# Performance work log

Hardware: AMD Instinct MI355X
Metric: run time of the kernel (lower is better)

The kernel has to match this reference:

```python
import jax, jax.numpy as jnp
import numpy as np
import math

N_NODES, N_EDGES, NNZ, D, L = 100000, 20000, 500000, 128, 4
ALPHA, LAMDA = 0.1, 0.5


def setup_inputs() -> dict:
    key = jax.random.key(0)
    ks = jax.random.split(key, 16)
    x = jax.random.normal(ks[0], (N_NODES, D), jnp.float32)
    e = jax.random.normal(ks[1], (N_EDGES, D), jnp.float32)
    nodes = jax.random.randint(ks[2], (NNZ,), 0, N_NODES)
    edges = jnp.sort(jax.random.randint(ks[3], (NNZ,), 0, N_EDGES)).at[-1].set(N_EDGES - 1)
    hyperedge_index = jnp.stack([nodes, edges]).astype(jnp.int32)
    dist_v2e = jax.random.randint(ks[4], (NNZ,), 0, 64).astype(jnp.float32)
    deg_v2e = jax.random.randint(ks[5], (NNZ,), 0, 64).astype(jnp.float32)
    dist_e2v = jax.random.randint(ks[6], (NNZ,), 0, 64).astype(jnp.float32)
    deg_e2v = jax.random.randint(ks[7], (NNZ,), 0, 64).astype(jnp.float32)
    s = 0.05
    W0 = jax.random.normal(ks[8], (D, D), jnp.float32) * s
    b0 = jnp.zeros((D,), jnp.float32)
    Wn = jax.random.normal(ks[9], (L, D, D), jnp.float32) * s
    We = jax.random.normal(ks[10], (L, D, D), jnp.float32) * s
    attn_w = jax.random.normal(ks[11], (L, 2 * D), jnp.float32) * s
    attn_b = jnp.zeros((L,), jnp.float32)
    wd_w = jax.random.normal(ks[12], (L,), jnp.float32) * s
    wd_b = jnp.zeros((L,), jnp.float32)
    wg_w = jax.random.normal(ks[13], (L,), jnp.float32) * s
    wg_b = jnp.zeros((L,), jnp.float32)
    return dict(x=x, e=e, hyperedge_index=hyperedge_index, dist_v2e=dist_v2e,
                deg_v2e=deg_v2e, dist_e2v=dist_e2v, deg_e2v=deg_e2v,
                W0=W0, b0=b0, Wn=Wn, We=We, attn_w=attn_w, attn_b=attn_b,
                wd_w=wd_w, wd_b=wd_b, wg_w=wg_w, wg_b=wg_b)


def _seg_softmax(s, idx, num):
    # numerically-stable scatter_softmax over segments idx
    m = jax.ops.segment_max(s, idx, num_segments=num)
    ex = jnp.exp(s - m[idx])
    den = jax.ops.segment_sum(ex, idx, num_segments=num)
    return ex / den[idx]


def _forward(x, e, hei, dv2e, gv2e, de2v, ge2v, W0, b0, Wn, We, aw, ab, wdw, wdb, wgw, wgb):
    nodes, edges = hei[0], hei[1]
    N, E = x.shape[0], e.shape[0]
    ones = jnp.ones(nodes.shape[0], x.dtype)
    dV = jax.ops.segment_sum(ones, nodes, num_segments=N)
    cnt = jax.ops.segment_sum(ones, edges, num_segments=E)
    dE = jax.ops.segment_sum(dV[nodes], edges, num_segments=E) / jnp.maximum(cnt, 1.0)
    degV = jnp.where(dV > 0, dV ** -0.5, 1.0)[:, None]   # [N,1]
    degE = jnp.where(dE > 0, dE ** -0.5, 1.0)[:, None]   # [E,1]

    x = jax.nn.relu(x @ W0 + b0)
    x0, e0 = x, e
    d = x.shape[1]
    for i in range(L):
        beta = math.log(LAMDA / (i + 1) + 1.0)
        # v2e attention: concat [x[nodes], e[edges]] -> softmax over edge segments
        sx1 = x @ aw[i, :d]; se1 = e @ aw[i, d:]
        s_v2e = sx1[nodes] + se1[edges] + ab[i] + dv2e * wdw[i] + wdb[i] + gv2e * wgw[i] + wgb[i]
        a_v2e = _seg_softmax(s_v2e, edges, E)[:, None]
        # e2v attention (flipped): concat [e[edges], x[nodes]] -> softmax over node segments
        se2 = e @ aw[i, :d]; sx2 = x @ aw[i, d:]
        s_e2v = se2[edges] + sx2[nodes] + ab[i] + de2v * wdw[i] + wdb[i] + ge2v * wgw[i] + wgb[i]
        a_e2v = _seg_softmax(s_e2v, nodes, N)[:, None]

        Xe1 = jax.ops.segment_sum(x[nodes] * a_v2e, edges, num_segments=E) * degE
        Xv1 = jax.ops.segment_sum(Xe1[edges] * a_e2v, nodes, num_segments=N) * degV
        Xv2 = jax.ops.segment_sum(e[edges] * a_e2v, nodes, num_segments=N) * degV
        Xe2 = jax.ops.segment_sum(Xv2[nodes] * a_v2e, edges, num_segments=E) * degE
        xm = (Xv1 + Xv2) * 0.5
        em = (Xe1 + Xe2) * 0.5
        xi = (1 - ALPHA) * xm + ALPHA * x0
        x = (1 - beta) * xi + beta * (xi @ Wn[i])
        ei = (1 - ALPHA) * em + ALPHA * e0
        e = (1 - beta) * ei + beta * (ei @ We[i])
        if i < L - 1:
            x = jax.nn.relu(x)
            e = jax.nn.relu(e)
    return x, e


def reference(x, e, hyperedge_index, dist_v2e, deg_v2e, dist_e2v, deg_e2v,
              W0, b0, Wn, We, attn_w, attn_b, wd_w, wd_b, wg_w, wg_b):
    return _forward(x, e, hyperedge_index, dist_v2e, deg_v2e, dist_e2v, deg_e2v,
                    W0, b0, Wn, We, attn_w, attn_b, wd_w, wd_b, wg_w, wg_b)
```

## Files before the change

kernel.cpp:

```cpp
#include <hip/hip_runtime.h>
#include <hip/hip_fp16.h>
#include <math.h>

#define DD 128
#define SCAN_BLOCKS 256

typedef _Float16 f16x8 __attribute__((ext_vector_type(8)));
typedef float f32x4 __attribute__((ext_vector_type(4)));

__device__ inline float wave_sum(float v){
#pragma unroll
  for (int m = 32; m >= 1; m >>= 1) v += __shfl_xor(v, m, 64);
  return v;
}
__device__ inline int wave_sum_i(int v){
#pragma unroll
  for (int m = 32; m >= 1; m >>= 1) v += __shfl_xor(v, m, 64);
  return v;
}


__global__ void k_edge_offsets(const int* __restrict__ edges, int nnz, int E,
                               int* __restrict__ eo){
  int e = blockIdx.x * blockDim.x + threadIdx.x;
  if (e > E) return;
  int lo = 0, hi = nnz;
  while (lo < hi){ int mid = (lo + hi) >> 1; if (edges[mid] < e) lo = mid + 1; else hi = mid; }
  eo[e] = lo;
}

__global__ void k_hist(const int* __restrict__ nodes, int nnz, int* __restrict__ dV){
  int k = blockIdx.x * blockDim.x + threadIdx.x;
  if (k < nnz) atomicAdd(&dV[nodes[k]], 1);
}

__global__ __launch_bounds__(256) void k_scan_partial(const int* __restrict__ dV, int N,
                                                      int* __restrict__ part){
  int b = blockIdx.x, t = threadIdx.x;
  int chunk = (N + SCAN_BLOCKS - 1) / SCAN_BLOCKS;
  int s0 = b * chunk, s1 = min(s0 + chunk, N);
  int sum = 0;
  for (int n = s0 + t; n < s1; n += 256) sum += dV[n];
  sum = wave_sum_i(sum);
  __shared__ int wred[4];
  int lane = t & 63, wid = t >> 6;
  if (lane == 0) wred[wid] = sum;
  __syncthreads();
  if (t == 0) part[b] = wred[0] + wred[1] + wred[2] + wred[3];
}

__global__ __launch_bounds__(SCAN_BLOCKS) void k_scan_blocksums(int* __restrict__ part){
  __shared__ int sh[SCAN_BLOCKS];
  int t = threadIdx.x;
  int v = part[t];
  sh[t] = v; __syncthreads();
  for (int off = 1; off < SCAN_BLOCKS; off <<= 1){
    int add = (t >= off) ? sh[t - off] : 0;
    __syncthreads();
    sh[t] += add;
    __syncthreads();
  }
  part[t] = sh[t] - v;
}

__global__ __launch_bounds__(256) void k_scan_apply(const int* __restrict__ dV, int N, int nnz,
    const int* __restrict__ partScan, int* __restrict__ no, int* __restrict__ nfill,
    float* __restrict__ degV){
  int b = blockIdx.x, t = threadIdx.x;
  int chunk = (N + SCAN_BLOCKS - 1) / SCAN_BLOCKS;
  int s0 = b * chunk, s1 = min(s0 + chunk, N);
  int lane = t & 63, wid = t >> 6;
  __shared__ int wtot[4];
  __shared__ int s_run;
  if (t == 0) s_run = partScan[b];
  __syncthreads();
  for (int base = s0; base < s1; base += 256){
    int n = base + t;
    int d = (n < s1) ? dV[n] : 0;
    int v = d;
#pragma unroll
    for (int off = 1; off < 64; off <<= 1){
      int o = __shfl_up(v, off, 64);
      if (lane >= off) v += o;
    }
    if (lane == 63) wtot[wid] = v;
    __syncthreads();
    int run0 = s_run;
    int woff = 0;
    for (int w = 0; w < wid; w++) woff += wtot[w];
    if (n < s1){
      int excl = run0 + woff + v - d;
      no[n] = excl; nfill[n] = excl;
      degV[n] = d > 0 ? 1.0f / sqrtf((float)d) : 1.0f;
    }
    int btot = wtot[0] + wtot[1] + wtot[2] + wtot[3];
    __syncthreads();
    if (t == 0) s_run = run0 + btot;
    __syncthreads();
  }
  if (b == 0 && t == 0) no[N] = nnz;
}

__global__ void k_perm(const int* __restrict__ nodes, int nnz,
                       int* __restrict__ nfill, int* __restrict__ perm){
  int k = blockIdx.x * blockDim.x + threadIdx.x;
  if (k < nnz){ int pos = atomicAdd(&nfill[nodes[k]], 1); perm[pos] = k; }
}

__global__ void k_pack(const int* __restrict__ perm, const int* __restrict__ edges,
                       const float* __restrict__ dist, const float* __restrict__ deg,
                       int nnz, float4* __restrict__ pack){
  int j = blockIdx.x * blockDim.x + threadIdx.x;
  if (j < nnz){
    int k = perm[j];
    pack[j] = make_float4(__int_as_float(edges[k]), dist[k], deg[k], 0.f);
  }
}

__global__ void k_edge_deg(const int* __restrict__ nodes, const int* __restrict__ eo, int E,
                           const int* __restrict__ dV, float* __restrict__ degE){
  int e = blockIdx.x * blockDim.x + threadIdx.x;
  if (e >= E) return;
  int b = eo[e], en = eo[e + 1];
  float s = 0.f;
  for (int k = b; k < en; k++) s += (float)dV[nodes[k]];
  float cnt = (float)(en - b);
  float dE = s / fmaxf(cnt, 1.0f);
  degE[e] = dE > 0.f ? 1.0f / sqrtf(dE) : 1.0f;
}

__global__ void k_tohalf(const float2* __restrict__ src, __half2* __restrict__ dst, int n){
  int i = blockIdx.x * blockDim.x + threadIdx.x;
  if (i < n){ float2 v = src[i]; dst[i] = __floats2half2_rn(v.x, v.y); }
}

__global__ __launch_bounds__(256) void k_einit(const float2* __restrict__ e_in2,
    const float* __restrict__ aw1, const float* __restrict__ aw2,
    int E, __half2* __restrict__ ET, float* __restrict__ se1, float* __restrict__ se2){
  int wave = threadIdx.x >> 6, lane = threadIdx.x & 63;
  int e = blockIdx.x * 4 + wave;
  if (e >= E) return;
  float2 v = e_in2[(size_t)e * 64 + lane];
  ET[(size_t)e * 128 + 2 * lane + 1] = __floats2half2_rn(v.x, v.y);
  float2 a2v = ((const float2*)aw2)[lane];
  float2 a1v = ((const float2*)aw1)[lane];
  float s1 = v.x * a2v.x + v.y * a2v.y;
  float s2 = v.x * a1v.x + v.y * a1v.y;
  s1 = wave_sum(s1); s2 = wave_sum(s2);
  if (lane == 0){ se1[e] = s1; se2[e] = s2; }
}

__global__ void k_wcast(const float* __restrict__ W0, const float* __restrict__ Wn,
                        const float* __restrict__ We, _Float16* __restrict__ Wt){
  int idx = blockIdx.x * 256 + threadIdx.x;
  if (idx >= 9 * 16384) return;
  int m = idx >> 14, r = idx & 16383;
  int n = r >> 7, k = r & 127;
  const float* src = (m == 0) ? W0 : (m <= 4 ? Wn + (size_t)(m - 1) * 16384
                                             : We + (size_t)(m - 5) * 16384);
  Wt[(size_t)m * 16384 + n * 128 + k] = (_Float16)src[k * 128 + n];
}


__global__ __launch_bounds__(256) void k_softmax_v2e(
    const int* __restrict__ nodes, const int* __restrict__ eo,
    const float* __restrict__ sx1, const float* __restrict__ se1,
    const float* __restrict__ dist, const float* __restrict__ deg,
    const float* __restrict__ ab, const float* __restrict__ wdw, const float* __restrict__ wdb,
    const float* __restrict__ wgw, const float* __restrict__ wgb, int li,
    const float* __restrict__ degE,
    int E, float* __restrict__ a_out, float* __restrict__ esc){
  int l32 = threadIdx.x & 31;
  int grp = threadIdx.x >> 5;
  int e = blockIdx.x * 8 + grp;
  if (e >= E) return;
  int b = eo[e], en = eo[e + 1];
  if (b >= en){ if (l32 == 0) esc[e] = 0.f; return; }
  float base = se1[e] + ab[li] + wdb[li] + wgb[li];
  float wd = wdw[li], wg = wgw[li];
  float m = -INFINITY;
  for (int k = b + l32; k < en; k += 32){
    float s = sx1[nodes[k]] + base + dist[k] * wd + deg[k] * wg;
    a_out[k] = s;
    m = fmaxf(m, s);
  }
#pragma unroll
  for (int mm = 16; mm >= 1; mm >>= 1) m = fmaxf(m, __shfl_xor(m, mm, 32));
  float sum = 0.f;
  for (int k = b + l32; k < en; k += 32){
    float ex = expf(a_out[k] - m);
    a_out[k] = ex; sum += ex;
  }
#pragma unroll
  for (int mm = 16; mm >= 1; mm >>= 1) sum += __shfl_xor(sum, mm, 32);
  if (l32 == 0) esc[e] = degE[e] / sum;
}

__device__ inline void acc8h(const float4 q, float w, float* a){
  float2 h0 = __half22float2(*(const __half2*)&q.x);
  float2 h1 = __half22float2(*(const __half2*)&q.y);
  float2 h2v = __half22float2(*(const __half2*)&q.z);
  float2 h3 = __half22float2(*(const __half2*)&q.w);
  a[0] += w * h0.x; a[1] += w * h0.y; a[2] += w * h1.x; a[3] += w * h1.y;
  a[4] += w * h2v.x; a[5] += w * h2v.y; a[6] += w * h3.x; a[7] += w * h3.y;
}

__global__ __launch_bounds__(256) void k_agg1(const int* __restrict__ nodes, const int* __restrict__ eo,
    const float4* __restrict__ xh4, const float* __restrict__ a_v2e, const float* __restrict__ esc,
    int E, __half2* __restrict__ ET){
  int l32 = threadIdx.x & 31;
  int grp = threadIdx.x >> 5;
  int e = blockIdx.x * 8 + grp;
  if (e >= E) return;
  int b = eo[e], en = eo[e + 1];
  int l16 = l32 & 15, hf = l32 >> 4;
  float a[8] = {0.f, 0.f, 0.f, 0.f, 0.f, 0.f, 0.f, 0.f};
  int k = b + hf;
  for (; k + 2 < en; k += 4){
    int n0 = nodes[k], n1 = nodes[k + 2];
    float w0 = a_v2e[k], w1 = a_v2e[k + 2];
    float4 v0 = xh4[(size_t)n0 * 16 + l16];
    float4 v1 = xh4[(size_t)n1 * 16 + l16];
    acc8h(v0, w0, a); acc8h(v1, w1, a);
  }
  for (; k < en; k += 2){
    int n = nodes[k];
    float w = a_v2e[k];
    float4 v = xh4[(size_t)n * 16 + l16];
    acc8h(v, w, a);
  }
#pragma unroll
  for (int j = 0; j < 8; j++) a[j] += __shfl_xor(a[j], 16, 32);
  if (hf == 0){
    float s = esc[e];
    size_t o = (size_t)e * 128 + 8 * l16;
    ET[o]     = __floats2half2_rn(a[0] * s, a[1] * s);
    ET[o + 2] = __floats2half2_rn(a[2] * s, a[3] * s);
    ET[o + 4] = __floats2half2_rn(a[4] * s, a[5] * s);
    ET[o + 6] = __floats2half2_rn(a[6] * s, a[7] * s);
  }
}

__device__ inline void acc8(const float4 q, float w, float* a1, float* a2){
  float2 x0 = __half22float2(*(const __half2*)&q.x);
  float2 e0 = __half22float2(*(const __half2*)&q.y);
  float2 x1 = __half22float2(*(const __half2*)&q.z);
  float2 e1 = __half22float2(*(const __half2*)&q.w);
  a1[0] += w * x0.x; a1[1] += w * x0.y; a1[2] += w * x1.x; a1[3] += w * x1.y;
  a2[0] += w * e0.x; a2[1] += w * e0.y; a2[2] += w * e1.x; a2[3] += w * e1.y;
}

__global__ __launch_bounds__(256) void k_agg2f(
    const float4* __restrict__ pack, const int* __restrict__ no,
    const float* __restrict__ se2, const float* __restrict__ sx2,
    const float* __restrict__ ab, const float* __restrict__ wdw, const float* __restrict__ wdb,
    const float* __restrict__ wgw, const float* __restrict__ wgb, int li,
    const float4* __restrict__ ETq,
    const float* __restrict__ degV, const __half2* __restrict__ x0h,
    int N, __half2* __restrict__ Xv2h, float* __restrict__ xi){
  int l32 = threadIdx.x & 31;
  int grp = threadIdx.x >> 5;
  int n = blockIdx.x * 8 + grp;
  if (n >= N) return;
  int b = no[n], en = no[n + 1];
  float base = sx2[n] + ab[li] + wdb[li] + wgb[li];
  float wd = wdw[li], wg = wgw[li];
  float m_run = -INFINITY, l_run = 0.f;
  float a1[4] = {0.f, 0.f, 0.f, 0.f}, a2[4] = {0.f, 0.f, 0.f, 0.f};
  for (int cb = b; cb < en; cb += 32){
    int cs = min(32, en - cb);
    float s = -INFINITY; int e_l = 0;
    if (l32 < cs){
      float4 pk = pack[cb + l32];
      e_l = __float_as_int(pk.x);
      s = se2[e_l] + base + pk.y * wd + pk.z * wg;
    }
    float m_c = s;
#pragma unroll
    for (int mm = 16; mm >= 1; mm >>= 1) m_c = fmaxf(m_c, __shfl_xor(m_c, mm, 32));
    float p = (l32 < cs) ? expf(s - m_c) : 0.f;
    float l_c = p;
#pragma unroll
    for (int mm = 16; mm >= 1; mm >>= 1) l_c += __shfl_xor(l_c, mm, 32);
    float m_new = fmaxf(m_run, m_c);
    float f_old = expf(m_run - m_new);
    float f_c = expf(m_c - m_new);
#pragma unroll
    for (int r = 0; r < 4; r++){ a1[r] *= f_old; a2[r] *= f_old; }
    l_run = l_run * f_old + l_c * f_c;
    m_run = m_new;
    int jj = 0;
    for (; jj + 3 < cs; jj += 4){
      float w0 = __shfl(p, jj, 32) * f_c;
      float w1 = __shfl(p, jj + 1, 32) * f_c;
      float w2 = __shfl(p, jj + 2, 32) * f_c;
      float w3 = __shfl(p, jj + 3, 32) * f_c;
      int e0i = __shfl(e_l, jj, 32);
      int e1i = __shfl(e_l, jj + 1, 32);
      int e2i = __shfl(e_l, jj + 2, 32);
      int e3i = __shfl(e_l, jj + 3, 32);
      float4 q0 = ETq[(size_t)e0i * 32 + l32];
      float4 q1 = ETq[(size_t)e1i * 32 + l32];
      float4 q2 = ETq[(size_t)e2i * 32 + l32];
      float4 q3 = ETq[(size_t)e3i * 32 + l32];
      acc8(q0, w0, a1, a2);
      acc8(q1, w1, a1, a2);
      acc8(q2, w2, a1, a2);
      acc8(q3, w3, a1, a2);
    }
    for (; jj < cs; jj++){
      float w = __shfl(p, jj, 32) * f_c;
      int ei_ = __shfl(e_l, jj, 32);
      float4 q = ETq[(size_t)ei_ * 32 + l32];
      acc8(q, w, a1, a2);
    }
  }
  float inv = l_run > 0.f ? 1.0f / l_run : 0.f;
  float dv = degV[n] * inv;
  float2 st;
  *(__half2*)&st.x = __floats2half2_rn(a2[0] * dv, a2[1] * dv);
  *(__half2*)&st.y = __floats2half2_rn(a2[2] * dv, a2[3] * dv);
  *(float2*)&Xv2h[(size_t)n * 64 + 2 * l32] = st;
  float2 x0v2 = *(const float2*)&x0h[(size_t)n * 64 + 2 * l32];
  float2 h0 = __half22float2(*(const __half2*)&x0v2.x);
  float2 h1 = __half22float2(*(const __half2*)&x0v2.y);
  float4 o;
  o.x = 0.45f * dv * (a1[0] + a2[0]) + 0.1f * h0.x;
  o.y = 0.45f * dv * (a1[1] + a2[1]) + 0.1f * h0.y;
  o.z = 0.45f * dv * (a1[2] + a2[2]) + 0.1f * h1.x;
  o.w = 0.45f * dv * (a1[3] + a2[3]) + 0.1f * h1.y;
  *(float4*)(xi + (size_t)n * 128 + 4 * l32) = o;
}

__global__ __launch_bounds__(256) void k_agg3(const int* __restrict__ nodes, const int* __restrict__ eo,
    const float4* __restrict__ Xv2h4, const float* __restrict__ a_v2e, const float* __restrict__ esc,
    const float4* __restrict__ ETq, const float* __restrict__ e0,
    int E, float* __restrict__ ei){
  int l32 = threadIdx.x & 31;
  int grp = threadIdx.x >> 5;
  int e = blockIdx.x * 8 + grp;
  if (e >= E) return;
  int b = eo[e], en = eo[e + 1];
  int l16 = l32 & 15, hf = l32 >> 4;
  float a[8] = {0.f, 0.f, 0.f, 0.f, 0.f, 0.f, 0.f, 0.f};
  int k = b + hf;
  for (; k + 2 < en; k += 4){
    int n0 = nodes[k], n1 = nodes[k + 2];
    float w0 = a_v2e[k], w1 = a_v2e[k + 2];
    float4 v0 = Xv2h4[(size_t)n0 * 16 + l16];
    float4 v1 = Xv2h4[(size_t)n1 * 16 + l16];
    acc8h(v0, w0, a); acc8h(v1, w1, a);
  }
  for (; k < en; k += 2){
    int n = nodes[k];
    float w = a_v2e[k];
    float4 v = Xv2h4[(size_t)n * 16 + l16];
    acc8h(v, w, a);
  }
#pragma unroll
  for (int j = 0; j < 8; j++) a[j] += __shfl_xor(a[j], 16, 32);
  if (hf == 0){
    float dE = esc[e];
    float4 q0 = ETq[(size_t)e * 32 + 2 * l16];
    float4 q1 = ETq[(size_t)e * 32 + 2 * l16 + 1];
    float2 x01 = __half22float2(*(const __half2*)&q0.x);
    float2 x23 = __half22float2(*(const __half2*)&q0.z);
    float2 x45 = __half22float2(*(const __half2*)&q1.x);
    float2 x67 = __half22float2(*(const __half2*)&q1.z);
    const float4* e04 = (const float4*)(e0 + (size_t)e * 128 + 8 * l16);
    float4 ev0 = e04[0], ev1 = e04[1];
    float4 o0, o1;
    o0.x = 0.45f * (x01.x + a[0] * dE) + 0.1f * ev0.x;
    o0.y = 0.45f * (x01.y + a[1] * dE) + 0.1f * ev0.y;
    o0.z = 0.45f * (x23.x + a[2] * dE) + 0.1f * ev0.z;
    o0.w = 0.45f * (x23.y + a[3] * dE) + 0.1f * ev0.w;
    o1.x = 0.45f * (x45.x + a[4] * dE) + 0.1f * ev1.x;
    o1.y = 0.45f * (x45.y + a[5] * dE) + 0.1f * ev1.y;
    o1.z = 0.45f * (x67.x + a[6] * dE) + 0.1f * ev1.z;
    o1.w = 0.45f * (x67.y + a[7] * dE) + 0.1f * ev1.w;
    float* eip = ei + (size_t)e * 128 + 8 * l16;
    *(float4*)eip = o0;
    *(float4*)(eip + 4) = o1;
  }
}

__global__ __launch_bounds__(256) void k_gemm_mfma(
    const _Float16* __restrict__ Ah, const _Float16* __restrict__ Wt,
    const float* __restrict__ Af, const float* __restrict__ bias,
    float* __restrict__ outf, _Float16* __restrict__ outh, _Float16* __restrict__ outh2, int et,
    const float* __restrict__ awA, const float* __restrict__ awB,
    float* __restrict__ sA, float* __restrict__ sB,
    int nrows, float beta, int mode, int do_relu){
  int wave = threadIdx.x >> 6, lane = threadIdx.x & 63;
  int row0 = blockIdx.x * 64 + wave * 16;
  if (row0 >= nrows) return;
  int lm = lane & 15;
  int lk8 = (lane >> 4) * 8;
  int arow = row0 + lm; if (arow >= nrows) arow = nrows - 1;
  f16x8 afrag[4];
  if (mode == 0){
#pragma unroll
    for (int ks = 0; ks < 4; ks++)
      afrag[ks] = *(const f16x8*)(Ah + (size_t)arow * 128 + ks * 32 + lk8);
  } else {
    const float* ap = Af + (size_t)arow * 128;
#pragma unroll
    for (int ks = 0; ks < 4; ks++){
      float4 v0 = *(const float4*)(ap + ks * 32 + lk8);
      float4 v1 = *(const float4*)(ap + ks * 32 + lk8 + 4);
      f16x8 a;
      a[0] = (_Float16)v0.x; a[1] = (_Float16)v0.y; a[2] = (_Float16)v0.z; a[3] = (_Float16)v0.w;
      a[4] = (_Float16)v1.x; a[5] = (_Float16)v1.y; a[6] = (_Float16)v1.z; a[7] = (_Float16)v1.w;
      afrag[ks] = a;
    }
  }
  int rbase = (lane >> 4) * 4;
  float da[4] = {0.f, 0.f, 0.f, 0.f}, db[4] = {0.f, 0.f, 0.f, 0.f};
  for (int t = 0; t < 8; t++){
    f32x4 acc = {0.f, 0.f, 0.f, 0.f};
#pragma unroll
    for (int ks = 0; ks < 4; ks++){
      f16x8 bf = *(const f16x8*)(Wt + (size_t)(t * 16 + lm) * 128 + ks * 32 + lk8);
      acc = __builtin_amdgcn_mfma_f32_16x16x32_f16(afrag[ks], bf, acc, 0, 0, 0);
    }
    int col = t * 16 + lm;
    float wa = 0.f, wb = 0.f;
    if (awA){ wa = awA[col]; wb = awB[col]; }
#pragma unroll
    for (int r = 0; r < 4; r++){
      int gr = row0 + rbase + r;
      if (gr >= nrows) continue;
      float v;
      if (mode == 0) v = acc[r] + bias[col];
      else v = (1.0f - beta) * Af[(size_t)gr * 128 + col] + beta * acc[r];
      if (do_relu) v = fmaxf(v, 0.f);
      if (outf) outf[(size_t)gr * 128 + col] = v;
      if (outh){
        if (et) outh[(size_t)gr * 256 + (col >> 1) * 4 + 2 + (col & 1)] = (_Float16)v;
        else    outh[(size_t)gr * 128 + col] = (_Float16)v;
      }
      if (outh2) outh2[(size_t)gr * 128 + col] = (_Float16)v;
      da[r] += v * wa; db[r] += v * wb;
    }
  }
  if (awA){
#pragma unroll
    for (int r = 0; r < 4; r++){
      float a = da[r], bb = db[r];
#pragma unroll
      for (int m = 8; m >= 1; m >>= 1){
        a += __shfl_xor(a, m, 64);
        bb += __shfl_xor(bb, m, 64);
      }
      int gr = row0 + rbase + r;
      if (lm == 0 && gr < nrows){ sA[gr] = a; sB[gr] = bb; }
    }
  }
}


extern "C" void kernel_launch(void* const* d_in, const int* in_sizes, int n_in,
                              void* d_out, int out_size, void* d_ws, size_t ws_size,
                              hipStream_t stream) {
  const float* x_in     = (const float*)d_in[0];
  const float* e_in     = (const float*)d_in[1];
  const int*   hei      = (const int*)d_in[2];
  const float* dist_v2e = (const float*)d_in[3];
  const float* deg_v2e  = (const float*)d_in[4];
  const float* dist_e2v = (const float*)d_in[5];
  const float* deg_e2v  = (const float*)d_in[6];
  const float* W0       = (const float*)d_in[7];
  const float* b0       = (const float*)d_in[8];
  const float* Wn       = (const float*)d_in[9];
  const float* We       = (const float*)d_in[10];
  const float* attn_w   = (const float*)d_in[11];
  const float* attn_b   = (const float*)d_in[12];
  const float* wd_w     = (const float*)d_in[13];
  const float* wd_b     = (const float*)d_in[14];
  const float* wg_w     = (const float*)d_in[15];
  const float* wg_b     = (const float*)d_in[16];

  const int N   = in_sizes[0] / DD;
  const int E   = in_sizes[1] / DD;
  const int NNZ = in_sizes[2] / 2;
  const int* nodesArr = hei;
  const int* edgesArr = hei + NNZ;

  float* out_x = (float*)d_out;
  float* out_e = (float*)d_out + (size_t)N * DD;

  __half2* Xv2h = (__half2*)out_x;
  __half2* xh   = (__half2*)((char*)out_x + (size_t)N * DD * 2);
  __half2* ET   = (__half2*)out_e;
  const float4* ETq = (const float4*)out_e;

  char* wsp = (char*)d_ws;
  auto alloc = [&](size_t bytes) -> void* {
    void* p = (void*)wsp;
    wsp += (bytes + 255) / 256 * 256;
    return p;
  };
  float* xS1   = (float*)alloc((size_t)N * DD * 4);
  float* eS1   = (float*)alloc((size_t)E * DD * 4);
  _Float16* xinh = (_Float16*)alloc((size_t)N * DD * 2);
  _Float16* x0h  = (_Float16*)alloc((size_t)N * DD * 2);
  _Float16* Wt   = (_Float16*)alloc((size_t)9 * 16384 * 2);
  float* sx1   = (float*)alloc((size_t)N * 4);
  float* sx2   = (float*)alloc((size_t)N * 4);
  float* se1   = (float*)alloc((size_t)E * 4);
  float* se2   = (float*)alloc((size_t)E * 4);
  float* a_v2e = (float*)alloc((size_t)NNZ * 4);
  float* degV  = (float*)alloc((size_t)N * 4);
  float* degE  = (float*)alloc((size_t)E * 4);
  float* esc   = (float*)alloc((size_t)E * 4);
  float4* pack = (float4*)alloc((size_t)NNZ * 16);
  int* dV_i  = (int*)alloc((size_t)N * 4);
  int* no_   = (int*)alloc((size_t)(N + 1) * 4);
  int* nfill = (int*)alloc((size_t)N * 4);
  int* perm  = (int*)alloc((size_t)NNZ * 4);
  int* eo    = (int*)alloc((size_t)(E + 1) * 4);
  int* part  = (int*)alloc((size_t)SCAN_BLOCKS * 4);

  hipMemsetAsync(dV_i, 0, (size_t)N * 4, stream);
  k_edge_offsets<<<(E + 1 + 255) / 256, 256, 0, stream>>>(edgesArr, NNZ, E, eo);
  k_hist<<<(NNZ + 255) / 256, 256, 0, stream>>>(nodesArr, NNZ, dV_i);
  k_scan_partial<<<SCAN_BLOCKS, 256, 0, stream>>>(dV_i, N, part);
  k_scan_blocksums<<<1, SCAN_BLOCKS, 0, stream>>>(part);
  k_scan_apply<<<SCAN_BLOCKS, 256, 0, stream>>>(dV_i, N, NNZ, part, no_, nfill, degV);
  k_perm<<<(NNZ + 255) / 256, 256, 0, stream>>>(nodesArr, NNZ, nfill, perm);
  k_pack<<<(NNZ + 255) / 256, 256, 0, stream>>>(perm, edgesArr, dist_e2v, deg_e2v, NNZ, pack);
  k_edge_deg<<<(E + 255) / 256, 256, 0, stream>>>(nodesArr, eo, E, dV_i, degE);
  k_wcast<<<(9 * 16384 + 255) / 256, 256, 0, stream>>>(W0, Wn, We, Wt);

  const float* aw1_0 = attn_w;
  const float* aw2_0 = attn_w + 128;

  k_einit<<<(E + 3) / 4, 256, 0, stream>>>((const float2*)e_in, aw1_0, aw2_0,
                                            E, ET, se1, se2);
  k_tohalf<<<((N * 64) + 255) / 256, 256, 0, stream>>>((const float2*)x_in, (__half2*)xinh, N * 64);

  k_gemm_mfma<<<(N + 63) / 64, 256, 0, stream>>>(xinh, Wt, nullptr, b0,
      nullptr, (_Float16*)xh, x0h, 0, aw1_0, aw2_0, sx1, sx2, N, 0.f, 0, 1);

  for (int i = 0; i < 4; i++){
    float beta = logf(0.5f / (float)(i + 1) + 1.0f);
    const float* aw1n = (i < 3) ? attn_w + (size_t)(i + 1) * 256        : nullptr;
    const float* aw2n = (i < 3) ? attn_w + (size_t)(i + 1) * 256 + 128  : nullptr;

    k_softmax_v2e<<<(E + 7) / 8, 256, 0, stream>>>(nodesArr, eo, sx1, se1,
        dist_v2e, deg_v2e, attn_b, wd_w, wd_b, wg_w, wg_b, i, degE, E, a_v2e, esc);

    k_agg1<<<(E + 7) / 8, 256, 0, stream>>>(nodesArr, eo, (const float4*)xh,
        a_v2e, esc, E, ET);
    k_agg2f<<<(N + 7) / 8, 256, 0, stream>>>(pack, no_, se2, sx2,
        attn_b, wd_w, wd_b, wg_w, wg_b, i,
        ETq, degV, (const __half2*)x0h, N, Xv2h, xS1);
    k_agg3<<<(E + 7) / 8, 256, 0, stream>>>(nodesArr, eo, (const float4*)Xv2h,
        a_v2e, esc, ETq, e_in, E, eS1);

    k_gemm_mfma<<<(N + 63) / 64, 256, 0, stream>>>(nullptr, Wt + (size_t)(1 + i) * 16384,
        xS1, nullptr, (i == 3) ? out_x : nullptr, (i < 3) ? (_Float16*)xh : nullptr,
        nullptr, 0, aw1n, aw2n, sx1, sx2, N, beta, 1, i < 3 ? 1 : 0);
    k_gemm_mfma<<<(E + 63) / 64, 256, 0, stream>>>(nullptr, Wt + (size_t)(5 + i) * 16384,
        eS1, nullptr, (i == 3) ? out_e : nullptr, (i < 3) ? (_Float16*)ET : nullptr,
        nullptr, 1, aw2n, aw1n, se1, se2, E, beta, 1, i < 3 ? 1 : 0);
  }
}
```

Baseline: 983.0 us.

## Fold beta residual into weights and store layer intermediates in half precision

The (1-beta)*xi + beta*xi@W blend is folded into the cast weight matrices as beta*W + (1-beta)*I. The GEMM no longer has to re-read the fp32 input row for the residual term. The aggregation kernels now write xi/ei and read e0 as fp16 instead of fp32, which halves the intermediate traffic and lets the GEMM load A fragments directly. The cost is extra fp16 rounding of the residual path and of the identity-augmented weights, which may reduce accuracy.

```diff
diff --git a/kernel.cpp b/kernel.cpp
--- a/kernel.cpp
+++ b/kernel.cpp
@@ -136,12 +136,15 @@
 
 __global__ __launch_bounds__(256) void k_einit(const float2* __restrict__ e_in2,
     const float* __restrict__ aw1, const float* __restrict__ aw2,
-    int E, __half2* __restrict__ ET, float* __restrict__ se1, float* __restrict__ se2){
+    int E, __half2* __restrict__ ET, __half2* __restrict__ e0h,
+    float* __restrict__ se1, float* __restrict__ se2){
   int wave = threadIdx.x >> 6, lane = threadIdx.x & 63;
   int e = blockIdx.x * 4 + wave;
   if (e >= E) return;
   float2 v = e_in2[(size_t)e * 64 + lane];
-  ET[(size_t)e * 128 + 2 * lane + 1] = __floats2half2_rn(v.x, v.y);
+  __half2 h = __floats2half2_rn(v.x, v.y);
+  ET[(size_t)e * 128 + 2 * lane + 1] = h;
+  e0h[(size_t)e * 64 + lane] = h;
   float2 a2v = ((const float2*)aw2)[lane];
   float2 a1v = ((const float2*)aw1)[lane];
   float s1 = v.x * a2v.x + v.y * a2v.y;
@@ -156,9 +159,16 @@
   if (idx >= 9 * 16384) return;
   int m = idx >> 14, r = idx & 16383;
   int n = r >> 7, k = r & 127;
-  const float* src = (m == 0) ? W0 : (m <= 4 ? Wn + (size_t)(m - 1) * 16384
-                                             : We + (size_t)(m - 5) * 16384);
-  Wt[(size_t)m * 16384 + n * 128 + k] = (_Float16)src[k * 128 + n];
+  float v;
+  if (m == 0){
+    v = W0[k * 128 + n];
+  } else {
+    int i = (m <= 4) ? m - 1 : m - 5;
+    const float* src = (m <= 4) ? Wn + (size_t)i * 16384 : We + (size_t)i * 16384;
+    float beta = logf(0.5f / (float)(i + 1) + 1.0f);
+    v = beta * src[k * 128 + n] + ((n == k) ? (1.0f - beta) : 0.f);
+  }
+  Wt[(size_t)m * 16384 + n * 128 + k] = (_Float16)v;
 }
 
 
@@ -257,7 +267,7 @@
     const float* __restrict__ wgw, const float* __restrict__ wgb, int li,
     const float4* __restrict__ ETq,
     const float* __restrict__ degV, const __half2* __restrict__ x0h,
-    int N, __half2* __restrict__ Xv2h, float* __restrict__ xi){
+    int N, __half2* __restrict__ Xv2h, __half2* __restrict__ xiH){
   int l32 = threadIdx.x & 31;
   int grp = threadIdx.x >> 5;
   int n = blockIdx.x * 8 + grp;
@@ -324,18 +334,18 @@
   float2 x0v2 = *(const float2*)&x0h[(size_t)n * 64 + 2 * l32];
   float2 h0 = __half22float2(*(const __half2*)&x0v2.x);
   float2 h1 = __half22float2(*(const __half2*)&x0v2.y);
-  float4 o;
-  o.x = 0.45f * dv * (a1[0] + a2[0]) + 0.1f * h0.x;
-  o.y = 0.45f * dv * (a1[1] + a2[1]) + 0.1f * h0.y;
-  o.z = 0.45f * dv * (a1[2] + a2[2]) + 0.1f * h1.x;
-  o.w = 0.45f * dv * (a1[3] + a2[3]) + 0.1f * h1.y;
-  *(float4*)(xi + (size_t)n * 128 + 4 * l32) = o;
+  float2 xo;
+  *(__half2*)&xo.x = __floats2half2_rn(0.45f * dv * (a1[0] + a2[0]) + 0.1f * h0.x,
+                                       0.45f * dv * (a1[1] + a2[1]) + 0.1f * h0.y);
+  *(__half2*)&xo.y = __floats2half2_rn(0.45f * dv * (a1[2] + a2[2]) + 0.1f * h1.x,
+                                       0.45f * dv * (a1[3] + a2[3]) + 0.1f * h1.y);
+  *(float2*)&xiH[(size_t)n * 64 + 2 * l32] = xo;
 }
 
 __global__ __launch_bounds__(256) void k_agg3(const int* __restrict__ nodes, const int* __restrict__ eo,
     const float4* __restrict__ Xv2h4, const float* __restrict__ a_v2e, const float* __restrict__ esc,
-    const float4* __restrict__ ETq, const float* __restrict__ e0,
-    int E, float* __restrict__ ei){
+    const float4* __restrict__ ETq, const float4* __restrict__ e0h4,
+    int E, __half2* __restrict__ eiH){
   int l32 = threadIdx.x & 31;
   int grp = threadIdx.x >> 5;
   int e = blockIdx.x * 8 + grp;
@@ -367,30 +377,31 @@
     float2 x23 = __half22float2(*(const __half2*)&q0.z);
     float2 x45 = __half22float2(*(const __half2*)&q1.x);
     float2 x67 = __half22float2(*(const __half2*)&q1.z);
-    const float4* e04 = (const float4*)(e0 + (size_t)e * 128 + 8 * l16);
-    float4 ev0 = e04[0], ev1 = e04[1];
-    float4 o0, o1;
-    o0.x = 0.45f * (x01.x + a[0] * dE) + 0.1f * ev0.x;
-    o0.y = 0.45f * (x01.y + a[1] * dE) + 0.1f * ev0.y;
-    o0.z = 0.45f * (x23.x + a[2] * dE) + 0.1f * ev0.z;
-    o0.w = 0.45f * (x23.y + a[3] * dE) + 0.1f * ev0.w;
-    o1.x = 0.45f * (x45.x + a[4] * dE) + 0.1f * ev1.x;
-    o1.y = 0.45f * (x45.y + a[5] * dE) + 0.1f * ev1.y;
-    o1.z = 0.45f * (x67.x + a[6] * dE) + 0.1f * ev1.z;
-    o1.w = 0.45f * (x67.y + a[7] * dE) + 0.1f * ev1.w;
-    float* eip = ei + (size_t)e * 128 + 8 * l16;
-    *(float4*)eip = o0;
-    *(float4*)(eip + 4) = o1;
+    float4 ev = e0h4[(size_t)e * 16 + l16];
+    float2 g0 = __half22float2(*(const __half2*)&ev.x);
+    float2 g1 = __half22float2(*(const __half2*)&ev.y);
+    float2 g2 = __half22float2(*(const __half2*)&ev.z);
+    float2 g3 = __half22float2(*(const __half2*)&ev.w);
+    float4 o;
+    *(__half2*)&o.x = __floats2half2_rn(0.45f * (x01.x + a[0] * dE) + 0.1f * g0.x,
+                                        0.45f * (x01.y + a[1] * dE) + 0.1f * g0.y);
+    *(__half2*)&o.y = __floats2half2_rn(0.45f * (x23.x + a[2] * dE) + 0.1f * g1.x,
+                                        0.45f * (x23.y + a[3] * dE) + 0.1f * g1.y);
+    *(__half2*)&o.z = __floats2half2_rn(0.45f * (x45.x + a[4] * dE) + 0.1f * g2.x,
+                                        0.45f * (x45.y + a[5] * dE) + 0.1f * g2.y);
+    *(__half2*)&o.w = __floats2half2_rn(0.45f * (x67.x + a[6] * dE) + 0.1f * g3.x,
+                                        0.45f * (x67.y + a[7] * dE) + 0.1f * g3.y);
+    *(float4*)&eiH[(size_t)e * 64 + 4 * l16] = o;
   }
 }
 
 __global__ __launch_bounds__(256) void k_gemm_mfma(
     const _Float16* __restrict__ Ah, const _Float16* __restrict__ Wt,
-    const float* __restrict__ Af, const float* __restrict__ bias,
+    const float* __restrict__ bias,
     float* __restrict__ outf, _Float16* __restrict__ outh, _Float16* __restrict__ outh2, int et,
     const float* __restrict__ awA, const float* __restrict__ awB,
     float* __restrict__ sA, float* __restrict__ sB,
-    int nrows, float beta, int mode, int do_relu){
+    int nrows, int do_relu){
   int wave = threadIdx.x >> 6, lane = threadIdx.x & 63;
   int row0 = blockIdx.x * 64 + wave * 16;
   if (row0 >= nrows) return;
@@ -398,22 +409,9 @@
   int lk8 = (lane >> 4) * 8;
   int arow = row0 + lm; if (arow >= nrows) arow = nrows - 1;
   f16x8 afrag[4];
-  if (mode == 0){
-#pragma unroll
-    for (int ks = 0; ks < 4; ks++)
-      afrag[ks] = *(const f16x8*)(Ah + (size_t)arow * 128 + ks * 32 + lk8);
-  } else {
-    const float* ap = Af + (size_t)arow * 128;
-#pragma unroll
-    for (int ks = 0; ks < 4; ks++){
-      float4 v0 = *(const float4*)(ap + ks * 32 + lk8);
-      float4 v1 = *(const float4*)(ap + ks * 32 + lk8 + 4);
-      f16x8 a;
-      a[0] = (_Float16)v0.x; a[1] = (_Float16)v0.y; a[2] = (_Float16)v0.z; a[3] = (_Float16)v0.w;
-      a[4] = (_Float16)v1.x; a[5] = (_Float16)v1.y; a[6] = (_Float16)v1.z; a[7] = (_Float16)v1.w;
-      afrag[ks] = a;
-    }
-  }
+#pragma unroll
+  for (int ks = 0; ks < 4; ks++)
+    afrag[ks] = *(const f16x8*)(Ah + (size_t)arow * 128 + ks * 32 + lk8);
   int rbase = (lane >> 4) * 4;
   float da[4] = {0.f, 0.f, 0.f, 0.f}, db[4] = {0.f, 0.f, 0.f, 0.f};
   for (int t = 0; t < 8; t++){
@@ -426,13 +424,12 @@
     int col = t * 16 + lm;
     float wa = 0.f, wb = 0.f;
     if (awA){ wa = awA[col]; wb = awB[col]; }
+    float bi = bias ? bias[col] : 0.f;
 #pragma unroll
     for (int r = 0; r < 4; r++){
       int gr = row0 + rbase + r;
       if (gr >= nrows) continue;
-      float v;
-      if (mode == 0) v = acc[r] + bias[col];
-      else v = (1.0f - beta) * Af[(size_t)gr * 128 + col] + beta * acc[r];
+      float v = acc[r] + bi;
       if (do_relu) v = fmaxf(v, 0.f);
       if (outf) outf[(size_t)gr * 128 + col] = v;
       if (outh){
@@ -500,10 +497,11 @@
     wsp += (bytes + 255) / 256 * 256;
     return p;
   };
-  float* xS1   = (float*)alloc((size_t)N * DD * 4);
-  float* eS1   = (float*)alloc((size_t)E * DD * 4);
   _Float16* xinh = (_Float16*)alloc((size_t)N * DD * 2);
   _Float16* x0h  = (_Float16*)alloc((size_t)N * DD * 2);
+  _Float16* xiH  = (_Float16*)alloc((size_t)N * DD * 2);
+  _Float16* eiH  = (_Float16*)alloc((size_t)E * DD * 2);
+  _Float16* e0h  = (_Float16*)alloc((size_t)E * DD * 2);
   _Float16* Wt   = (_Float16*)alloc((size_t)9 * 16384 * 2);
   float* sx1   = (float*)alloc((size_t)N * 4);
   float* sx2   = (float*)alloc((size_t)N * 4);
@@ -536,14 +534,13 @@
   const float* aw2_0 = attn_w + 128;
 
   k_einit<<<(E + 3) / 4, 256, 0, stream>>>((const float2*)e_in, aw1_0, aw2_0,
-                                            E, ET, se1, se2);
+                                            E, ET, (__half2*)e0h, se1, se2);
   k_tohalf<<<((N * 64) + 255) / 256, 256, 0, stream>>>((const float2*)x_in, (__half2*)xinh, N * 64);
 
-  k_gemm_mfma<<<(N + 63) / 64, 256, 0, stream>>>(xinh, Wt, nullptr, b0,
-      nullptr, (_Float16*)xh, x0h, 0, aw1_0, aw2_0, sx1, sx2, N, 0.f, 0, 1);
+  k_gemm_mfma<<<(N + 63) / 64, 256, 0, stream>>>(xinh, Wt, b0,
+      nullptr, (_Float16*)xh, x0h, 0, aw1_0, aw2_0, sx1, sx2, N, 1);
 
   for (int i = 0; i < 4; i++){
-    float beta = logf(0.5f / (float)(i + 1) + 1.0f);
     const float* aw1n = (i < 3) ? attn_w + (size_t)(i + 1) * 256        : nullptr;
     const float* aw2n = (i < 3) ? attn_w + (size_t)(i + 1) * 256 + 128  : nullptr;
 
@@ -554,15 +551,15 @@
         a_v2e, esc, E, ET);
     k_agg2f<<<(N + 7) / 8, 256, 0, stream>>>(pack, no_, se2, sx2,
         attn_b, wd_w, wd_b, wg_w, wg_b, i,
-        ETq, degV, (const __half2*)x0h, N, Xv2h, xS1);
+        ETq, degV, (const __half2*)x0h, N, Xv2h, (__half2*)xiH);
     k_agg3<<<(E + 7) / 8, 256, 0, stream>>>(nodesArr, eo, (const float4*)Xv2h,
-        a_v2e, esc, ETq, e_in, E, eS1);
-
-    k_gemm_mfma<<<(N + 63) / 64, 256, 0, stream>>>(nullptr, Wt + (size_t)(1 + i) * 16384,
-        xS1, nullptr, (i == 3) ? out_x : nullptr, (i < 3) ? (_Float16*)xh : nullptr,
-        nullptr, 0, aw1n, aw2n, sx1, sx2, N, beta, 1, i < 3 ? 1 : 0);
-    k_gemm_mfma<<<(E + 63) / 64, 256, 0, stream>>>(nullptr, Wt + (size_t)(5 + i) * 16384,
-        eS1, nullptr, (i == 3) ? out_e : nullptr, (i < 3) ? (_Float16*)ET : nullptr,
-        nullptr, 1, aw2n, aw1n, se1, se2, E, beta, 1, i < 3 ? 1 : 0);
-  }
-}
+        a_v2e, esc, ETq, (const float4*)e0h, E, (__half2*)eiH);
+
+    k_gemm_mfma<<<(N + 63) / 64, 256, 0, stream>>>(xiH, Wt + (size_t)(1 + i) * 16384,
+        nullptr, (i == 3) ? out_x : nullptr, (i < 3) ? (_Float16*)xh : nullptr,
+        nullptr, 0, aw1n, aw2n, sx1, sx2, N, i < 3 ? 1 : 0);
+    k_gemm_mfma<<<(E + 63) / 64, 256, 0, stream>>>(eiH, Wt + (size_t)(5 + i) * 16384,
+        nullptr, (i == 3) ? out_e : nullptr, (i < 3) ? (_Float16*)ET : nullptr,
+        nullptr, 1, aw2n, aw1n, se1, se2, E, i < 3 ? 1 : 0);
+  }
+}
```

Measured after the change: 926.5 us. 1.06x faster.
